# Kernel tuning notes

Hardware: AMD Instinct MI355X
Metric: run time of the kernel (lower is better)

## Reference

```python
import jax, jax.numpy as jnp
import numpy as np

B, S, C = 4, 2048, 1024
H = 16
D = C // H  # head_dim = 64


def setup_inputs() -> dict:
    key = jax.random.key(0)
    ks = jax.random.split(key, 5)
    scale = 0.02
    return {
        "x": jax.random.normal(ks[0], (B, S, C), dtype=jnp.float32),
        "qkv_w": jax.random.normal(ks[1], (3 * C, C), dtype=jnp.float32) * scale,
        "qkv_b": jax.random.normal(ks[2], (3 * C,), dtype=jnp.float32) * scale,
        "proj_w": jax.random.normal(ks[3], (C, C), dtype=jnp.float32) * scale,
        "proj_b": jax.random.normal(ks[4], (C,), dtype=jnp.float32) * scale,
    }


def reference(x, qkv_w, qkv_b, proj_w, proj_b):
    b, s, c = x.shape
    qkv = x @ qkv_w.T + qkv_b            # [b,s,3c] (torch Linear: x W^T + b)
    q, k, v = jnp.split(qkv, 3, axis=2)
    # [b,s,c] -> [b,h,s,d]
    def heads(t):
        return t.reshape(b, s, H, D).transpose(0, 2, 1, 3)
    q, k, v = heads(q), heads(k), heads(v)
    scores = jnp.einsum("bhqd,bhkd->bhqk", q, k) / jnp.sqrt(jnp.float32(D))
    causal = jnp.tril(jnp.ones((s, s), dtype=bool))
    scores = jnp.where(causal[None, None], scores, -jnp.inf)
    weights = jax.nn.softmax(scores, axis=-1)
    out = jnp.einsum("bhqk,bhkd->bhqd", weights, v)
    out = out.transpose(0, 2, 1, 3).reshape(b, s, c)
    return out @ proj_w.T + proj_b
```

## Files before the change

kernel.cpp:

```cpp
#include <hip/hip_runtime.h>
#include <hip/hip_bf16.h>


typedef __attribute__((ext_vector_type(8))) short short8;
typedef __attribute__((ext_vector_type(4))) float floatx4;

__device__ __forceinline__ unsigned short f2b(float f) {
    union { float f; unsigned u; } x; x.f = f;
    unsigned r = (x.u + 0x7fffu + ((x.u >> 16) & 1u)) >> 16;
    return (unsigned short)r;
}

__device__ __forceinline__ void load16_to_lds(const unsigned short* g, unsigned short* l) {
    auto gp = (const __attribute__((address_space(1))) unsigned int*)(unsigned long long)g;
    auto lp = (__attribute__((address_space(3))) unsigned int*)(unsigned int)(unsigned long long)l;
    __builtin_amdgcn_global_load_lds(gp, lp, 16, 0, 0);
}

__global__ void __launch_bounds__(256)
convert_all(const float* __restrict__ x, const float* __restrict__ w1,
            const float* __restrict__ w2, unsigned short* __restrict__ xb,
            unsigned short* __restrict__ wb1, unsigned short* __restrict__ wb2) {
    const int N0 = 2097152, N1 = 786432;
    int i = blockIdx.x * 256 + threadIdx.x;
    const float* src; unsigned short* dst; int off;
    if (i < N0)           { src = x;  dst = xb;  off = i; }
    else if (i < N0 + N1) { src = w1; dst = wb1; off = i - N0; }
    else                  { src = w2; dst = wb2; off = i - N0 - N1; }
    float4 f = ((const float4*)src)[off];
    ushort4 u;
    u.x = f2b(f.x); u.y = f2b(f.y); u.z = f2b(f.z); u.w = f2b(f.w);
    ((ushort4*)dst)[off] = u;
}

template<int MODE>
__global__ void __launch_bounds__(256)
gemm_nt(const unsigned short* __restrict__ A, const unsigned short* __restrict__ Bw,
        const float* __restrict__ bias, int M, int N, int K,
        unsigned short* __restrict__ Qo, unsigned short* __restrict__ Ko,
        unsigned short* __restrict__ Vo, float* __restrict__ Co) {
    __shared__ unsigned short As[128][64];
    __shared__ unsigned short Bs[128][64];
    const int tid = threadIdx.x;
    const int wave = tid >> 6, lane = tid & 63;
    const int lane15 = lane & 15, quad = lane >> 4;
    const int waveM = wave >> 1, waveN = wave & 1;
    const int m0 = blockIdx.y * 128, n0 = blockIdx.x * 128;
    const int swz = (lane15 & 7);

    floatx4 acc[4][4];
#pragma unroll
    for (int i = 0; i < 4; ++i)
#pragma unroll
        for (int j = 0; j < 4; ++j) acc[i][j] = (floatx4){0.f, 0.f, 0.f, 0.f};

    for (int kt = 0; kt < K; kt += 64) {
        __syncthreads();
#pragma unroll
        for (int i = 0; i < 4; ++i) {
            int idx = tid + i * 256;
            int r = idx >> 3, c = idx & 7;
            int gc = (c ^ (r & 7)) * 8;
            load16_to_lds(&A[(size_t)(m0 + r) * K + kt + gc], &As[0][0] + idx * 8);
            load16_to_lds(&Bw[(size_t)(n0 + r) * K + kt + gc], &Bs[0][0] + idx * 8);
        }
        __asm__ volatile("s_waitcnt vmcnt(0)" ::: "memory");
        __syncthreads();
#pragma unroll
        for (int ks = 0; ks < 2; ++ks) {
            short8 af[4], bfr[4];
#pragma unroll
            for (int i = 0; i < 4; ++i)
                af[i] = *(const short8*)&As[waveM * 64 + i * 16 + lane15][((ks * 4 + quad) ^ swz) * 8];
#pragma unroll
            for (int j = 0; j < 4; ++j)
                bfr[j] = *(const short8*)&Bs[waveN * 64 + j * 16 + lane15][((ks * 4 + quad) ^ swz) * 8];
#pragma unroll
            for (int i = 0; i < 4; ++i)
#pragma unroll
                for (int j = 0; j < 4; ++j)
                    acc[i][j] = __builtin_amdgcn_mfma_f32_16x16x32_bf16(af[i], bfr[j], acc[i][j], 0, 0, 0);
        }
    }

    const float QSCALE = 0.18033688011112042f;
    if (MODE == 0) {
        const int sel = n0 >> 10;
#pragma unroll
        for (int i = 0; i < 4; ++i)
#pragma unroll
            for (int j = 0; j < 4; ++j) {
                const int n = n0 + waveN * 64 + j * 16 + lane15;
                const int c = n & 1023;
                const int h = c >> 6, d = c & 63;
                const float bia = bias[n];
                const int mbase = m0 + waveM * 64 + i * 16 + quad * 4;
                const int b = mbase >> 11, s = mbase & 2047;
                const size_t bh = (size_t)(b * 16 + h);
                if (sel == 2) {
                    ushort4 w;
                    w.x = f2b(acc[i][j][0] + bia);
                    w.y = f2b(acc[i][j][1] + bia);
                    w.z = f2b(acc[i][j][2] + bia);
                    w.w = f2b(acc[i][j][3] + bia);
                    *(ushort4*)&Vo[(bh * 64 + d) * 2048 + s] = w;
                } else {
                    unsigned short* dst = (sel == 0) ? Qo : Ko;
                    const float sc = (sel == 0) ? QSCALE : 1.0f;
#pragma unroll
                    for (int r = 0; r < 4; ++r)
                        dst[(bh * 2048 + s + r) * 64 + d] = f2b((acc[i][j][r] + bia) * sc);
                }
            }
    } else {
#pragma unroll
        for (int i = 0; i < 4; ++i)
#pragma unroll
            for (int j = 0; j < 4; ++j)
#pragma unroll
                for (int r = 0; r < 4; ++r) {
                    int m = m0 + waveM * 64 + i * 16 + quad * 4 + r;
                    int n = n0 + waveN * 64 + j * 16 + lane15;
                    Co[(size_t)m * N + n] = acc[i][j][r] + bias[n];
                }
    }
}

__global__ void __launch_bounds__(256, 2)
attn_kernel(const unsigned short* __restrict__ Q, const unsigned short* __restrict__ K,
            const unsigned short* __restrict__ V, unsigned short* __restrict__ O) {
    const int S = 2048, D = 64;
    __shared__ unsigned short Ks[2][64][64];
    __shared__ unsigned short Vt[2][64][64];
    __shared__ __align__(16) unsigned short Ps[4][32][72];

    const int flat = blockIdx.y * 8 + blockIdx.x;
    const int xcd = flat & 7, slot = flat >> 3;
    const int bh = xcd * 8 + (slot & 7);
    const int bx = slot >> 3;

    const int tid = threadIdx.x;
    const int wave = tid >> 6, lane = tid & 63;
    const int lane15 = lane & 15, quad = lane >> 4;
    const int swz = (lane15 & 7);

    const unsigned short* Qb = Q + (size_t)bh * S * D;
    const unsigned short* Kb = K + (size_t)bh * S * D;
    const unsigned short* Vb = V + (size_t)bh * D * S;
    const int b = bh >> 4, h = bh & 15;

    auto stage = [&](int buf, int kb) {
#pragma unroll
        for (int i = 0; i < 2; ++i) {
            int idx = tid + i * 256;
            int r = idx >> 3, c = idx & 7;
            int gc = (c ^ (r & 7)) * 8;
            load16_to_lds(&Kb[(size_t)(kb + r) * D + gc], &Ks[buf][0][0] + idx * 8);
            load16_to_lds(&Vb[(size_t)r * S + kb + gc], &Vt[buf][0][0] + idx * 8);
        }
    };

    for (int qi = 0; qi < 2; ++qi) {
        const int qb = qi ? bx : 15 - bx;
        const int q0 = qb * 128;
        const int ntiles = 2 * qb + 2;

        short8 qf[2][2];
#pragma unroll
        for (int mi = 0; mi < 2; ++mi) {
            int qrow = q0 + wave * 32 + mi * 16 + lane15;
#pragma unroll
            for (int ks = 0; ks < 2; ++ks)
                qf[mi][ks] = *(const short8*)&Qb[(size_t)qrow * D + ks * 32 + quad * 8];
        }

        floatx4 o[2][4];
        float l_acc[2];
#pragma unroll
        for (int mi = 0; mi < 2; ++mi) {
            l_acc[mi] = 0.f;
#pragma unroll
            for (int r = 0; r < 4; ++r) o[mi][r] = (floatx4){0.f, 0.f, 0.f, 0.f};
        }

        __syncthreads();
        stage(0, 0);

        for (int kt = 0; kt < ntiles; ++kt) {
            const int cur = kt & 1;
            const int kb = kt * 64;
            __asm__ volatile("s_waitcnt vmcnt(0)" ::: "memory");
            __syncthreads();
            if (kt + 1 < ntiles) stage(1 - cur, kb + 64);

            floatx4 sa[2][4];
#pragma unroll
            for (int mi = 0; mi < 2; ++mi)
#pragma unroll
                for (int j = 0; j < 4; ++j) sa[mi][j] = (floatx4){0.f, 0.f, 0.f, 0.f};
#pragma unroll
            for (int j = 0; j < 4; ++j)
#pragma unroll
                for (int ks = 0; ks < 2; ++ks) {
                    short8 kf = *(const short8*)&Ks[cur][j * 16 + lane15][((ks * 4 + quad) ^ swz) * 8];
#pragma unroll
                    for (int mi = 0; mi < 2; ++mi)
                        sa[mi][j] = __builtin_amdgcn_mfma_f32_16x16x32_bf16(kf, qf[mi][ks], sa[mi][j], 0, 0, 0);
                }

            if (kb + 64 > q0) {
#pragma unroll
                for (int mi = 0; mi < 2; ++mi)
#pragma unroll
                    for (int j = 0; j < 4; ++j)
#pragma unroll
                        for (int r = 0; r < 4; ++r) {
                            int key = kb + j * 16 + quad * 4 + r;
                            int qq = q0 + wave * 32 + mi * 16 + lane15;
                            if (key > qq) sa[mi][j][r] = -1e30f;
                        }
            }

#pragma unroll
            for (int mi = 0; mi < 2; ++mi) {
#pragma unroll
                for (int j = 0; j < 4; ++j)
#pragma unroll
                    for (int r = 0; r < 4; ++r)
                        sa[mi][j][r] = __builtin_amdgcn_exp2f(sa[mi][j][r]);
#pragma unroll
                for (int j = 0; j < 4; ++j)
                    l_acc[mi] += (sa[mi][j][0] + sa[mi][j][1]) + (sa[mi][j][2] + sa[mi][j][3]);
#pragma unroll
                for (int j = 0; j < 4; ++j) {
                    unsigned w0, w1;
                    __asm__("v_cvt_pk_bf16_f32 %0, %1, %2"
                            : "=v"(w0) : "v"(sa[mi][j][0]), "v"(sa[mi][j][1]));
                    __asm__("v_cvt_pk_bf16_f32 %0, %1, %2"
                            : "=v"(w1) : "v"(sa[mi][j][2]), "v"(sa[mi][j][3]));
                    uint2 w; w.x = w0; w.y = w1;
                    *(uint2*)&Ps[wave][mi * 16 + lane15][j * 16 + quad * 4] = w;
                }
            }
            __asm__ volatile("s_waitcnt lgkmcnt(0)" ::: "memory");

            short8 pf[2][2];
#pragma unroll
            for (int mi = 0; mi < 2; ++mi)
#pragma unroll
                for (int ks = 0; ks < 2; ++ks)
                    pf[mi][ks] = *(const short8*)&Ps[wave][mi * 16 + lane15][ks * 32 + quad * 8];

#pragma unroll
            for (int jd = 0; jd < 4; ++jd)
#pragma unroll
                for (int ks = 0; ks < 2; ++ks) {
                    short8 vf = *(const short8*)&Vt[cur][jd * 16 + lane15][((ks * 4 + quad) ^ swz) * 8];
#pragma unroll
                    for (int mi = 0; mi < 2; ++mi)
                        o[mi][jd] = __builtin_amdgcn_mfma_f32_16x16x32_bf16(pf[mi][ks], vf, o[mi][jd], 0, 0, 0);
                }
        }

#pragma unroll
        for (int mi = 0; mi < 2; ++mi) {
            l_acc[mi] += __shfl_xor(l_acc[mi], 16);
            l_acc[mi] += __shfl_xor(l_acc[mi], 32);
        }

#pragma unroll
        for (int mi = 0; mi < 2; ++mi)
#pragma unroll
            for (int r = 0; r < 4; ++r) {
                int qq = q0 + wave * 32 + mi * 16 + quad * 4 + r;
                float lq = __shfl(l_acc[mi], (lane & 48) + quad * 4 + r);
                float inv = 1.0f / lq;
#pragma unroll
                for (int jd = 0; jd < 4; ++jd)
                    O[((size_t)(b * 2048 + qq)) * 1024 + h * 64 + jd * 16 + lane15] =
                        f2b(o[mi][jd][r] * inv);
            }
    }
}

extern "C" void kernel_launch(void* const* d_in, const int* in_sizes, int n_in,
                              void* d_out, int out_size, void* d_ws, size_t ws_size,
                              hipStream_t stream) {
    const float* x      = (const float*)d_in[0];
    const float* qkv_w  = (const float*)d_in[1];
    const float* qkv_b  = (const float*)d_in[2];
    const float* proj_w = (const float*)d_in[3];
    const float* proj_b = (const float*)d_in[4];
    float* out = (float*)d_out;

    const int B = 4, S = 2048, C = 1024, M = B * S;

    char* ws = (char*)d_ws;
    size_t off = 0;
    auto alloc = [&](size_t bytes) {
        void* p = ws + off;
        off += (bytes + 255) & ~(size_t)255;
        return p;
    };
    unsigned short* xb    = (unsigned short*)alloc((size_t)M * C * 2);
    unsigned short* wqkv  = (unsigned short*)alloc((size_t)3 * C * C * 2);
    unsigned short* wproj = (unsigned short*)alloc((size_t)C * C * 2);
    unsigned short* Qb    = (unsigned short*)alloc((size_t)M * C * 2);
    unsigned short* Kb    = (unsigned short*)alloc((size_t)M * C * 2);
    unsigned short* Vb    = (unsigned short*)alloc((size_t)M * C * 2);
    unsigned short* attn  = (unsigned short*)alloc((size_t)M * C * 2);

    {
        int total4 = (M * C + 3 * C * C + C * C) / 4;
        convert_all<<<total4 / 256, 256, 0, stream>>>(x, qkv_w, proj_w, xb, wqkv, wproj);
    }

    gemm_nt<0><<<dim3(3 * C / 128, M / 128), 256, 0, stream>>>(
        xb, wqkv, qkv_b, M, 3 * C, C, Qb, Kb, Vb, nullptr);

    attn_kernel<<<dim3(8, B * 16), 256, 0, stream>>>(Qb, Kb, Vb, attn);

    gemm_nt<1><<<dim3(C / 128, M / 128), 256, 0, stream>>>(
        attn, wproj, proj_b, M, C, C, nullptr, nullptr, nullptr, out);
}
```

Measured before the change: 233.4 us.

## Add 256x256 double-buffered pipelined QKV GEMM kernel with 8 waves

Replaces the 128x128 single-buffered QKV projection GEMM with a dedicated 256x256-tile, 512-thread kernel. It double-buffers LDS, issues global-to-LDS async loads in quarter-tile stages interleaved with MFMA phases, and uses s_setprio to favour math. The larger tile improves operand reuse and the pipelining hides load latency behind compute. In exchange it uses 128KB of LDS per block (limiting occupancy) and the grid shrinks to 384 blocks, which may cause tail imbalance across CUs.

```diff
diff --git a/kernel.cpp b/kernel.cpp
--- a/kernel.cpp
+++ b/kernel.cpp
@@ -33,12 +33,166 @@
     ((ushort4*)dst)[off] = u;
 }
 
-template<int MODE>
+__global__ void __launch_bounds__(512, 2)
+gemm_qkv_256(const unsigned short* __restrict__ A, const unsigned short* __restrict__ Bw,
+             const float* __restrict__ bias,
+             unsigned short* __restrict__ Qo, unsigned short* __restrict__ Ko,
+             unsigned short* __restrict__ Vo) {
+    const int K = 1024;
+    __shared__ unsigned short As[2][256][64];
+    __shared__ unsigned short Bs[2][256][64];
+    const int tid = threadIdx.x;
+    const int wave = tid >> 6, lane = tid & 63;
+    const int lane15 = lane & 15, quad = lane >> 4;
+    const int wr = wave >> 2, wc = wave & 3;
+    const int m0 = blockIdx.y * 256, n0 = blockIdx.x * 256;
+    const int swz = lane15 & 7;
+
+    auto stage = [&](int h) {
+        const int tile = h >> 2, part = h & 3;
+        const int buf = tile & 1, kt = tile * 64;
+        const int hh = part & 1;
+        const bool isA = part >= 2;
+        const unsigned short* src = isA ? A : Bw;
+        const int r0 = (isA ? m0 : n0) + hh * 128;
+        unsigned short* dst = isA ? &As[buf][hh * 128][0] : &Bs[buf][hh * 128][0];
+#pragma unroll
+        for (int i = 0; i < 2; ++i) {
+            int idx = tid + i * 512;
+            int r = idx >> 3, c = idx & 7;
+            int gc = (c ^ (r & 7)) * 8;
+            load16_to_lds(&src[(size_t)(r0 + r) * K + kt + gc], dst + idx * 8);
+        }
+    };
+
+    floatx4 acc[8][4];
+#pragma unroll
+    for (int i = 0; i < 8; ++i)
+#pragma unroll
+        for (int j = 0; j < 4; ++j) acc[i][j] = (floatx4){0.f, 0.f, 0.f, 0.f};
+
+#pragma unroll
+    for (int h = 0; h < 6; ++h) stage(h);
+    __asm__ volatile("s_waitcnt vmcnt(4)" ::: "memory");
+    __builtin_amdgcn_s_barrier();
+
+    short8 af[4][2], b0[2][2], b1[2][2];
+    for (int t = 0; t < 16; ++t) {
+        const int cur = t & 1;
+        const int s0 = 4 * t;
+
+#pragma unroll
+        for (int m = 0; m < 4; ++m)
+#pragma unroll
+            for (int ks = 0; ks < 2; ++ks)
+                af[m][ks] = *(const short8*)&As[cur][wr * 128 + m * 16 + lane15][((ks * 4 + quad) ^ swz) * 8];
+#pragma unroll
+        for (int n = 0; n < 2; ++n)
+#pragma unroll
+            for (int ks = 0; ks < 2; ++ks)
+                b0[n][ks] = *(const short8*)&Bs[cur][wc * 64 + n * 16 + lane15][((ks * 4 + quad) ^ swz) * 8];
+        if (s0 + 6 < 64) stage(s0 + 6);
+        __builtin_amdgcn_s_barrier();
+        __builtin_amdgcn_s_setprio(1);
+#pragma unroll
+        for (int m = 0; m < 4; ++m)
+#pragma unroll
+            for (int n = 0; n < 2; ++n)
+#pragma unroll
+                for (int ks = 0; ks < 2; ++ks)
+                    acc[m][n] = __builtin_amdgcn_mfma_f32_16x16x32_bf16(af[m][ks], b0[n][ks], acc[m][n], 0, 0, 0);
+        __builtin_amdgcn_s_setprio(0);
+        __builtin_amdgcn_s_barrier();
+
+#pragma unroll
+        for (int n = 0; n < 2; ++n)
+#pragma unroll
+            for (int ks = 0; ks < 2; ++ks)
+                b1[n][ks] = *(const short8*)&Bs[cur][wc * 64 + (n + 2) * 16 + lane15][((ks * 4 + quad) ^ swz) * 8];
+        if (s0 + 7 < 64) stage(s0 + 7);
+        __builtin_amdgcn_s_barrier();
+        __builtin_amdgcn_s_setprio(1);
+#pragma unroll
+        for (int m = 0; m < 4; ++m)
+#pragma unroll
+            for (int n = 0; n < 2; ++n)
+#pragma unroll
+                for (int ks = 0; ks < 2; ++ks)
+                    acc[m][n + 2] = __builtin_amdgcn_mfma_f32_16x16x32_bf16(af[m][ks], b1[n][ks], acc[m][n + 2], 0, 0, 0);
+        __builtin_amdgcn_s_setprio(0);
+        __builtin_amdgcn_s_barrier();
+
+#pragma unroll
+        for (int m = 0; m < 4; ++m)
+#pragma unroll
+            for (int ks = 0; ks < 2; ++ks)
+                af[m][ks] = *(const short8*)&As[cur][wr * 128 + (m + 4) * 16 + lane15][((ks * 4 + quad) ^ swz) * 8];
+        if (s0 + 8 < 64) stage(s0 + 8);
+        __builtin_amdgcn_s_barrier();
+        __builtin_amdgcn_s_setprio(1);
+#pragma unroll
+        for (int m = 0; m < 4; ++m)
+#pragma unroll
+            for (int n = 0; n < 2; ++n)
+#pragma unroll
+                for (int ks = 0; ks < 2; ++ks)
+                    acc[m + 4][n] = __builtin_amdgcn_mfma_f32_16x16x32_bf16(af[m][ks], b0[n][ks], acc[m + 4][n], 0, 0, 0);
+        __builtin_amdgcn_s_setprio(0);
+        __builtin_amdgcn_s_barrier();
+
+        if (s0 + 9 < 64) stage(s0 + 9);
+        if (t < 14)
+            __asm__ volatile("s_waitcnt vmcnt(4)" ::: "memory");
+        else if (t == 14)
+            __asm__ volatile("s_waitcnt vmcnt(0)" ::: "memory");
+        __builtin_amdgcn_s_barrier();
+        __builtin_amdgcn_s_setprio(1);
+#pragma unroll
+        for (int m = 0; m < 4; ++m)
+#pragma unroll
+            for (int n = 0; n < 2; ++n)
+#pragma unroll
+                for (int ks = 0; ks < 2; ++ks)
+                    acc[m + 4][n + 2] = __builtin_amdgcn_mfma_f32_16x16x32_bf16(af[m][ks], b1[n][ks], acc[m + 4][n + 2], 0, 0, 0);
+        __builtin_amdgcn_s_setprio(0);
+        __builtin_amdgcn_s_barrier();
+    }
+
+    const float QSCALE = 0.18033688011112042f;
+    const int sel = n0 >> 10;
+#pragma unroll
+    for (int nf = 0; nf < 4; ++nf) {
+        const int n = n0 + wc * 64 + nf * 16 + lane15;
+        const int c = n & 1023;
+        const int h = c >> 6, d = c & 63;
+        const float bia = bias[n];
+#pragma unroll
+        for (int mf = 0; mf < 8; ++mf) {
+            const int mbase = m0 + wr * 128 + mf * 16 + quad * 4;
+            const int b = mbase >> 11, s = mbase & 2047;
+            const size_t bh = (size_t)(b * 16 + h);
+            if (sel == 2) {
+                ushort4 w;
+                w.x = f2b(acc[mf][nf][0] + bia);
+                w.y = f2b(acc[mf][nf][1] + bia);
+                w.z = f2b(acc[mf][nf][2] + bia);
+                w.w = f2b(acc[mf][nf][3] + bia);
+                *(ushort4*)&Vo[(bh * 64 + d) * 2048 + s] = w;
+            } else {
+                unsigned short* dst = (sel == 0) ? Qo : Ko;
+                const float sc = (sel == 0) ? QSCALE : 1.0f;
+#pragma unroll
+                for (int r = 0; r < 4; ++r)
+                    dst[(bh * 2048 + s + r) * 64 + d] = f2b((acc[mf][nf][r] + bia) * sc);
+            }
+        }
+    }
+}
+
 __global__ void __launch_bounds__(256)
 gemm_nt(const unsigned short* __restrict__ A, const unsigned short* __restrict__ Bw,
         const float* __restrict__ bias, int M, int N, int K,
-        unsigned short* __restrict__ Qo, unsigned short* __restrict__ Ko,
-        unsigned short* __restrict__ Vo, float* __restrict__ Co) {
+        float* __restrict__ Co) {
     __shared__ unsigned short As[128][64];
     __shared__ unsigned short Bs[128][64];
     const int tid = threadIdx.x;
@@ -83,47 +237,16 @@
         }
     }
 
-    const float QSCALE = 0.18033688011112042f;
-    if (MODE == 0) {
-        const int sel = n0 >> 10;
-#pragma unroll
-        for (int i = 0; i < 4; ++i)
-#pragma unroll
-            for (int j = 0; j < 4; ++j) {
-                const int n = n0 + waveN * 64 + j * 16 + lane15;
-                const int c = n & 1023;
-                const int h = c >> 6, d = c & 63;
-                const float bia = bias[n];
-                const int mbase = m0 + waveM * 64 + i * 16 + quad * 4;
-                const int b = mbase >> 11, s = mbase & 2047;
-                const size_t bh = (size_t)(b * 16 + h);
-                if (sel == 2) {
-                    ushort4 w;
-                    w.x = f2b(acc[i][j][0] + bia);
-                    w.y = f2b(acc[i][j][1] + bia);
-                    w.z = f2b(acc[i][j][2] + bia);
-                    w.w = f2b(acc[i][j][3] + bia);
-                    *(ushort4*)&Vo[(bh * 64 + d) * 2048 + s] = w;
-                } else {
-                    unsigned short* dst = (sel == 0) ? Qo : Ko;
-                    const float sc = (sel == 0) ? QSCALE : 1.0f;
-#pragma unroll
-                    for (int r = 0; r < 4; ++r)
-                        dst[(bh * 2048 + s + r) * 64 + d] = f2b((acc[i][j][r] + bia) * sc);
-                }
+#pragma unroll
+    for (int i = 0; i < 4; ++i)
+#pragma unroll
+        for (int j = 0; j < 4; ++j)
+#pragma unroll
+            for (int r = 0; r < 4; ++r) {
+                int m = m0 + waveM * 64 + i * 16 + quad * 4 + r;
+                int n = n0 + waveN * 64 + j * 16 + lane15;
+                Co[(size_t)m * N + n] = acc[i][j][r] + bias[n];
             }
-    } else {
-#pragma unroll
-        for (int i = 0; i < 4; ++i)
-#pragma unroll
-            for (int j = 0; j < 4; ++j)
-#pragma unroll
-                for (int r = 0; r < 4; ++r) {
-                    int m = m0 + waveM * 64 + i * 16 + quad * 4 + r;
-                    int n = n0 + waveN * 64 + j * 16 + lane15;
-                    Co[(size_t)m * N + n] = acc[i][j][r] + bias[n];
-                }
-    }
 }
 
 __global__ void __launch_bounds__(256, 2)
@@ -315,11 +438,11 @@
         convert_all<<<total4 / 256, 256, 0, stream>>>(x, qkv_w, proj_w, xb, wqkv, wproj);
     }
 
-    gemm_nt<0><<<dim3(3 * C / 128, M / 128), 256, 0, stream>>>(
-        xb, wqkv, qkv_b, M, 3 * C, C, Qb, Kb, Vb, nullptr);
+    gemm_qkv_256<<<dim3(3 * C / 256, M / 256), 512, 0, stream>>>(
+        xb, wqkv, qkv_b, Qb, Kb, Vb);
 
     attn_kernel<<<dim3(8, B * 16), 256, 0, stream>>>(Qb, Kb, Vb, attn);
 
-    gemm_nt<1><<<dim3(C / 128, M / 128), 256, 0, stream>>>(
-        attn, wproj, proj_b, M, C, C, nullptr, nullptr, nullptr, out);
-}
+    gemm_nt<<<dim3(C / 128, M / 128), 256, 0, stream>>>(
+        attn, wproj, proj_b, M, C, C, out);
+}
```

Result: slower. 246.5 us (+5.6%).
